# Kernel tuning notes

Hardware: AMD Instinct MI355X
Metric: run time of the kernel (lower is better)

## Reference

```python
import jax, jax.numpy as jnp
import numpy as np

B, L, D = 4, 2048, 512
H, DK, DV = 8, 64, 64


def setup_inputs() -> dict:
    key = jax.random.key(0)
    ks = jax.random.split(key, 12)
    s = 0.02
    return {
        "query": jax.random.normal(ks[0], (B, L, D), jnp.float32),
        "key": jax.random.normal(ks[1], (B, L, D), jnp.float32),
        "value": jax.random.normal(ks[2], (B, L, D), jnp.float32),
        "attention_mask": jax.random.normal(ks[3], (1, 1, L, L), jnp.float32),
        "Wq": jax.random.normal(ks[4], (D, H * DK), jnp.float32) * s,
        "bq": jnp.zeros((H * DK,), jnp.float32),
        "Wk": jax.random.normal(ks[5], (D, H * DK), jnp.float32) * s,
        "bk": jnp.zeros((H * DK,), jnp.float32),
        "Wv": jax.random.normal(ks[6], (D, H * DV), jnp.float32) * s,
        "bv": jnp.zeros((H * DV,), jnp.float32),
        "Wo": jax.random.normal(ks[7], (H * DV, D), jnp.float32) * s,
        "bo": jnp.zeros((D,), jnp.float32),
    }


def reference(query, key, value, attention_mask, Wq, bq, Wk, bk, Wv, bv, Wo, bo):
    sz_b, len_q, _ = query.shape
    len_k = key.shape[1]
    # projections -> [B, L, H, d]
    q = (query @ Wq + bq).reshape(sz_b, len_q, H, DK)
    k = (key @ Wk + bk).reshape(sz_b, len_k, H, DK)
    v = (value @ Wv + bv).reshape(sz_b, len_k, H, DV)
    # permute(2,0,1,3): heads first -> [H, B, L, d]
    q = jnp.transpose(q, (2, 0, 1, 3))
    k = jnp.transpose(k, (2, 0, 1, 3))
    v = jnp.transpose(v, (2, 0, 1, 3))
    scale = 1.0 / jnp.sqrt(jnp.asarray(DK, q.dtype))
    scores = jnp.einsum('hbqd,hbkd->hbqk', q, k) * scale + attention_mask
    attn = jax.nn.softmax(scores, axis=-1)
    x = jnp.einsum('hbqk,hbkd->hbqd', attn, v)  # [H, B, Lq, Dv]
    # faithful to torch: transpose(1,2) -> [H, Lq, B, Dv] then view(B, Lq, H*Dv)
    x = jnp.transpose(x, (0, 2, 1, 3)).reshape(sz_b, len_q, H * DV)
    return x @ Wo + bo
```

## Files before the change

### kernel.cpp

```cpp
#include <hip/hip_runtime.h>

#define SEQ    2048
#define DMODEL 512
#define NHEAD  8
#define HDIM   64
#define BATCH  4
#define NROWS  65536
#define KSPLIT 2

#define LOG2E  1.4426950408889634f
#define QSCALE 0.18033688011112042f

typedef float f32x4  __attribute__((ext_vector_type(4)));
typedef float f32x16 __attribute__((ext_vector_type(16)));
typedef _Float16 h16x8 __attribute__((ext_vector_type(8)));
typedef _Float16 h16x2 __attribute__((ext_vector_type(2)));

union U4H { uint4 u; h16x8 h; };
union U1H2 { unsigned int u; h16x2 h; };

static __device__ inline h16x2 pkrtz(float a, float b) {
    return __builtin_bit_cast(h16x2, __builtin_amdgcn_cvt_pkrtz(a, b));
}
static __device__ inline unsigned short f2h(float x) {
    _Float16 h = (_Float16)x;
    return __builtin_bit_cast(unsigned short, h);
}
static __device__ inline void async_cp16(const void* g, void* l) {
    __builtin_amdgcn_global_load_lds(
        (const __attribute__((address_space(1))) unsigned int*)g,
        (__attribute__((address_space(3))) unsigned int*)l,
        16, 0, 0);
}

__global__ __launch_bounds__(256) void transpose_cast_w(
    const float* __restrict__ s0, const float* __restrict__ s1,
    const float* __restrict__ s2, const float* __restrict__ s3,
    unsigned short* __restrict__ d0, unsigned short* __restrict__ d1,
    unsigned short* __restrict__ d2, unsigned short* __restrict__ d3)
{
    const float* S; unsigned short* D;
    switch (blockIdx.z) {
        case 0: S = s0; D = d0; break;
        case 1: S = s1; D = d1; break;
        case 2: S = s2; D = d2; break;
        default: S = s3; D = d3; break;
    }
    __shared__ float T[32][33];
    const int t = threadIdx.x;
    const int r = t >> 3, c = (t & 7) * 4;
    const int k0 = blockIdx.x * 32, n0 = blockIdx.y * 32;
    float4 v = *(const float4*)&S[(size_t)(k0 + r) * DMODEL + n0 + c];
    T[r][c] = v.x; T[r][c + 1] = v.y; T[r][c + 2] = v.z; T[r][c + 3] = v.w;
    __syncthreads();
    ushort4 o;
    o.x = f2h(T[c + 0][r]); o.y = f2h(T[c + 1][r]);
    o.z = f2h(T[c + 2][r]); o.w = f2h(T[c + 3][r]);
    *(ushort4*)&D[(size_t)(n0 + r) * DMODEL + k0 + c] = o;
}

__global__ __launch_bounds__(256) void prep_mask(
    const float* __restrict__ mask, unsigned short* __restrict__ mp)
{
    int i = blockIdx.x * 256 + threadIdx.x;
    int k = (i * 4) & (SEQ - 1);
    int q = (i * 4) >> 11;
    float4 v = ((const float4*)mask)[i];
    int kt = k >> 6, kl = k & 63;
    int mt = kl >> 5, g = (kl >> 3) & 3, hl = (kl >> 2) & 1;
    size_t base = ((size_t)kt * SEQ + q) * 64 + hl * 32 + mt * 16 + g * 4;
    ushort4 o;
    o.x = f2h(__builtin_amdgcn_exp2f(v.x * LOG2E));
    o.y = f2h(__builtin_amdgcn_exp2f(v.y * LOG2E));
    o.z = f2h(__builtin_amdgcn_exp2f(v.z * LOG2E));
    o.w = f2h(__builtin_amdgcn_exp2f(v.w * LOG2E));
    *(ushort4*)&mp[base] = o;
}

template <int A_FP32, int EPI>
static __device__ inline void gemm_core(
    const void* __restrict__ Ap, const unsigned short* __restrict__ Bt,
    const float* __restrict__ bias, void* __restrict__ Cout, float oscale,
    int bm, int bn)
{
    __shared__ __align__(16) unsigned short As[128 * 32];
    __shared__ __align__(16) unsigned short Bs[128 * 32];

    const int t = threadIdx.x;
    const int lane = t & 63, w = t >> 6;
    const int wm = w >> 1, wn = w & 1;
    const int c = lane & 15, quad = lane >> 4;

    f32x4 acc[4][4] = {};

    for (int k0 = 0; k0 < DMODEL; k0 += 32) {
        if (A_FP32) {
            const float* Af = (const float*)Ap;
            #pragma unroll
            for (int p = 0; p < 4; p++) {
                int cid = p * 256 + t;
                int row = cid >> 3, fc = cid & 7;
                float4 av = *(const float4*)&Af[(size_t)(bm + row) * DMODEL + k0 + fc * 4];
                U1H2 lo, hi;
                lo.h = pkrtz(av.x, av.y);
                hi.h = pkrtz(av.z, av.w);
                uint2 st = make_uint2(lo.u, hi.u);
                *(uint2*)&As[row * 32 + fc * 4] = st;
            }
        } else {
            const unsigned short* Ab = (const unsigned short*)Ap;
            #pragma unroll
            for (int i = 0; i < 2; i++) {
                int row = 32 * w + 16 * i + (lane >> 2);
                const unsigned short* gp = Ab + (size_t)(bm + row) * DMODEL + k0 + (lane & 3) * 8;
                async_cp16(gp, &As[(32 * w + 16 * i) * 32]);
            }
        }
        #pragma unroll
        for (int i = 0; i < 2; i++) {
            int row = 32 * w + 16 * i + (lane >> 2);
            const unsigned short* gp = Bt + (size_t)(bn + row) * DMODEL + k0 + (lane & 3) * 8;
            async_cp16(gp, &Bs[(32 * w + 16 * i) * 32]);
        }
        __syncthreads();

        U4H af[4], bf[4];
        #pragma unroll
        for (int mt = 0; mt < 4; mt++)
            af[mt].u = *(const uint4*)&As[(wm * 64 + mt * 16 + c) * 32 + quad * 8];
        #pragma unroll
        for (int nt = 0; nt < 4; nt++)
            bf[nt].u = *(const uint4*)&Bs[(wn * 64 + nt * 16 + c) * 32 + quad * 8];
        #pragma unroll
        for (int mt = 0; mt < 4; mt++)
            #pragma unroll
            for (int nt = 0; nt < 4; nt++)
                acc[mt][nt] = __builtin_amdgcn_mfma_f32_16x16x32_f16(
                    af[mt].h, bf[nt].h, acc[mt][nt], 0, 0, 0);
        __syncthreads();
    }

    if (EPI == 2) {
        #pragma unroll
        for (int nt = 0; nt < 4; nt++) {
            int ng = bn + wn * 64 + nt * 16 + c;
            int h = ng >> 6, dv = ng & 63;
            float bv = bias[ng];
            #pragma unroll
            for (int mt = 0; mt < 4; mt++) {
                int mg0 = bm + wm * 64 + mt * 16 + quad * 4;
                int bb = mg0 >> 11, key0 = mg0 & (SEQ - 1);
                U1H2 lo, hi;
                lo.h = pkrtz(acc[mt][nt][0] + bv, acc[mt][nt][1] + bv);
                hi.h = pkrtz(acc[mt][nt][2] + bv, acc[mt][nt][3] + bv);
                *(uint2*)&((unsigned short*)Cout)[
                    ((size_t)(bb * NHEAD + h) * HDIM + dv) * SEQ + key0] =
                    make_uint2(lo.u, hi.u);
            }
        }
        return;
    }
    #pragma unroll
    for (int nt = 0; nt < 4; nt++) {
        int ng = bn + wn * 64 + nt * 16 + c;
        float bv = bias[ng];
        #pragma unroll
        for (int mt = 0; mt < 4; mt++) {
            #pragma unroll
            for (int r = 0; r < 4; r++) {
                int mg = bm + wm * 64 + mt * 16 + quad * 4 + r;
                float v = (acc[mt][nt][r] + bv) * oscale;
                if (EPI == 1)
                    ((unsigned short*)Cout)[(size_t)mg * DMODEL + ng] = f2h(v);
                else
                    ((float*)Cout)[(size_t)mg * DMODEL + ng] = v;
            }
        }
    }
}

struct QKVArgs {
    const float *A0, *A1, *A2;
    const unsigned short *W0, *W1, *W2;
    const float *b0, *b1, *b2;
    unsigned short *o0, *o1, *o2;
};

__global__ __launch_bounds__(256) void gemm_qkv(QKVArgs a) {
    if (blockIdx.z == 2)
        gemm_core<1, 2>(a.A2, a.W2, a.b2, a.o2, 1.0f, blockIdx.y * 128, blockIdx.x * 128);
    else if (blockIdx.z == 1)
        gemm_core<1, 1>(a.A1, a.W1, a.b1, a.o1, 1.0f, blockIdx.y * 128, blockIdx.x * 128);
    else
        gemm_core<1, 1>(a.A0, a.W0, a.b0, a.o0, QSCALE, blockIdx.y * 128, blockIdx.x * 128);
}

__global__ __launch_bounds__(256) void gemm_fin(
    const unsigned short* __restrict__ A, const unsigned short* __restrict__ W,
    const float* __restrict__ bias, float* __restrict__ C) {
    gemm_core<0, 0>(A, W, bias, C, 1.0f, blockIdx.y * 128, blockIdx.x * 128);
}

__global__ __launch_bounds__(256, 3) void attn5(
    const unsigned short* __restrict__ qb, const unsigned short* __restrict__ kb,
    const unsigned short* __restrict__ vT, const unsigned short* __restrict__ emp,
    unsigned short* __restrict__ Xp, float* __restrict__ Lp)
{
    __shared__ __align__(16) unsigned short Ks[2][64 * 64];
    __shared__ __align__(16) unsigned short Vs[2][64 * 64];

    const int t = threadIdx.x;
    const int lane = t & 63, w = t >> 6;
    const int c32 = lane & 31, hl = lane >> 5;
    const int bh = blockIdx.x, b = bh >> 3, head = bh & 7;
    const int q0 = blockIdx.y * 128;
    const int split = blockIdx.z;
    const int qg = q0 + w * 32 + c32;

    const unsigned short* qrow = qb + ((size_t)b * SEQ + qg) * DMODEL + head * HDIM;
    U4H Qf[4];
    #pragma unroll
    for (int s = 0; s < 4; s++)
        Qf[s].u = *(const uint4*)&qrow[s * 16 + hl * 8];

    const unsigned short* kgb = kb + (size_t)b * SEQ * DMODEL + head * HDIM
                              + (size_t)split * 1024 * DMODEL;
    const unsigned short* vgb = vT + (size_t)bh * HDIM * SEQ + split * 1024;

    const int srow = lane >> 3;
    const int sch  = (lane & 7) ^ srow;

    {
        #pragma unroll
        for (int i = 0; i < 2; i++) {
            int row = w * 16 + i * 8 + srow;
            async_cp16(&kgb[(size_t)row * DMODEL + sch * 8], &Ks[0][(w * 16 + i * 8) * 64]);
            async_cp16(&vgb[(size_t)row * SEQ + sch * 8],    &Vs[0][(w * 16 + i * 8) * 64]);
        }
    }

    f32x16 O0 = {}, O1 = {};
    float lsum = 0.f;

    for (int kt = 0; kt < 1024 / 64; kt++) {
        const int p = kt & 1;
        __syncthreads();

        const int ktg = split * 16 + kt;
        const unsigned short* mrow = emp + ((size_t)ktg * SEQ + qg) * 64 + hl * 32;
        U4H e0, e1, e2, e3;
        e0.u = *(const uint4*)&mrow[0];
        e1.u = *(const uint4*)&mrow[8];
        e2.u = *(const uint4*)&mrow[16];
        e3.u = *(const uint4*)&mrow[24];

        if (kt + 1 < 1024 / 64) {
            int k0n = (kt + 1) * 64;
            #pragma unroll
            for (int i = 0; i < 2; i++) {
                int row = w * 16 + i * 8 + srow;
                async_cp16(&kgb[(size_t)(k0n + row) * DMODEL + sch * 8],
                           &Ks[p ^ 1][(w * 16 + i * 8) * 64]);
                async_cp16(&vgb[(size_t)row * SEQ + k0n + sch * 8],
                           &Vs[p ^ 1][(w * 16 + i * 8) * 64]);
            }
        }

        const unsigned short* Kp = Ks[p];
        const unsigned short* Vp = Vs[p];

        f32x16 S0 = {}, S1 = {};
        #pragma unroll
        for (int s = 0; s < 4; s++) {
            int fc = 2 * s + hl;
            int sl = (fc ^ (c32 & 7)) * 8;
            U4H ka0, ka1;
            ka0.u = *(const uint4*)&Kp[c32 * 64 + sl];
            ka1.u = *(const uint4*)&Kp[(32 + c32) * 64 + sl];
            S0 = __builtin_amdgcn_mfma_f32_32x32x16_f16(ka0.h, Qf[s].h, S0, 0, 0, 0);
            S1 = __builtin_amdgcn_mfma_f32_32x32x16_f16(ka1.h, Qf[s].h, S1, 0, 0, 0);
        }

        unsigned int Pf[4][4];
        #pragma unroll
        for (int mt = 0; mt < 2; mt++) {
            f32x16 S = mt ? S1 : S0;
            h16x8 ea = (mt ? e2 : e0).h;
            h16x8 eb = (mt ? e3 : e1).h;
            unsigned int u[4][2];
            #pragma unroll
            for (int jj = 0; jj < 8; jj++) {
                _Float16 exl = (jj < 4) ? ea[2 * jj]     : eb[2 * jj - 8];
                _Float16 exh = (jj < 4) ? ea[2 * jj + 1] : eb[2 * jj - 7];
                h16x2 ex = {exl, exh};
                h16x2 pk = pkrtz(__builtin_amdgcn_exp2f(S[2 * jj]),
                                 __builtin_amdgcn_exp2f(S[2 * jj + 1]));
                h16x2 pp = pk * ex;
                lsum += (float)pp[0] + (float)pp[1];
                u[jj >> 1][jj & 1] = __builtin_bit_cast(unsigned int, pp);
            }
            unsigned int sA0 = hl ? u[0][0] : u[1][0];
            unsigned int sA1 = hl ? u[0][1] : u[1][1];
            unsigned int sB0 = hl ? u[2][0] : u[3][0];
            unsigned int sB1 = hl ? u[2][1] : u[3][1];
            unsigned int rA0 = (unsigned)__shfl_xor((int)sA0, 32, 64);
            unsigned int rA1 = (unsigned)__shfl_xor((int)sA1, 32, 64);
            unsigned int rB0 = (unsigned)__shfl_xor((int)sB0, 32, 64);
            unsigned int rB1 = (unsigned)__shfl_xor((int)sB1, 32, 64);
            Pf[2 * mt + 0][0] = hl ? rA0 : u[0][0];
            Pf[2 * mt + 0][1] = hl ? rA1 : u[0][1];
            Pf[2 * mt + 0][2] = hl ? u[1][0] : rA0;
            Pf[2 * mt + 0][3] = hl ? u[1][1] : rA1;
            Pf[2 * mt + 1][0] = hl ? rB0 : u[2][0];
            Pf[2 * mt + 1][1] = hl ? rB1 : u[2][1];
            Pf[2 * mt + 1][2] = hl ? u[3][0] : rB0;
            Pf[2 * mt + 1][3] = hl ? u[3][1] : rB1;
        }

        #pragma unroll
        for (int s = 0; s < 4; s++) {
            int kc = 2 * s + hl;
            int sl = (kc ^ (c32 & 7)) * 8;
            U4H va0, va1, pu;
            va0.u = *(const uint4*)&Vp[c32 * 64 + sl];
            va1.u = *(const uint4*)&Vp[(32 + c32) * 64 + sl];
            pu.u = make_uint4(Pf[s][0], Pf[s][1], Pf[s][2], Pf[s][3]);
            O0 = __builtin_amdgcn_mfma_f32_32x32x16_f16(va0.h, pu.h, O0, 0, 0, 0);
            O1 = __builtin_amdgcn_mfma_f32_32x32x16_f16(va1.h, pu.h, O1, 0, 0, 0);
        }
    }

    lsum += __shfl_xor(lsum, 32, 64);
    const size_t j = ((size_t)head * SEQ + qg) * BATCH + b;
    unsigned short* xr = Xp + ((size_t)split * NROWS + j) * HDIM;
    #pragma unroll
    for (int mt = 0; mt < 2; mt++) {
        f32x16 Ov = mt ? O1 : O0;
        #pragma unroll
        for (int g = 0; g < 4; g++) {
            U1H2 lo, hi;
            lo.h = pkrtz(Ov[g * 4 + 0], Ov[g * 4 + 1]);
            hi.h = pkrtz(Ov[g * 4 + 2], Ov[g * 4 + 3]);
            uint2 st = make_uint2(lo.u, hi.u);
            *(uint2*)&xr[mt * 32 + 8 * g + 4 * hl] = st;
        }
    }
    if (hl == 0) Lp[split * NROWS + j] = lsum;
}

__global__ __launch_bounds__(256) void combine_attn(
    const unsigned short* __restrict__ Xp, const float* __restrict__ Lp,
    unsigned short* __restrict__ xb)
{
    int i = blockIdx.x * 256 + threadIdx.x;
    int j = i >> 3, dc = (i & 7) * 8;
    U4H a, b;
    a.u = *(const uint4*)&Xp[(size_t)j * HDIM + dc];
    b.u = *(const uint4*)&Xp[((size_t)NROWS + j) * HDIM + dc];
    float inv = 1.0f / (Lp[j] + Lp[NROWS + j]);
    U4H o;
    #pragma unroll
    for (int p = 0; p < 4; p++) {
        float s0 = ((float)a.h[2 * p]     + (float)b.h[2 * p])     * inv;
        float s1 = ((float)a.h[2 * p + 1] + (float)b.h[2 * p + 1]) * inv;
        h16x2 pk = pkrtz(s0, s1);
        o.h[2 * p] = pk[0]; o.h[2 * p + 1] = pk[1];
    }
    *(uint4*)&xb[(size_t)j * HDIM + dc] = o.u;
}

extern "C" void kernel_launch(void* const* d_in, const int* in_sizes, int n_in,
                              void* d_out, int out_size, void* d_ws, size_t ws_size,
                              hipStream_t stream) {
    const float* query = (const float*)d_in[0];
    const float* key_  = (const float*)d_in[1];
    const float* value = (const float*)d_in[2];
    const float* mask  = (const float*)d_in[3];
    const float* Wq = (const float*)d_in[4];
    const float* bq = (const float*)d_in[5];
    const float* Wk = (const float*)d_in[6];
    const float* bk = (const float*)d_in[7];
    const float* Wv = (const float*)d_in[8];
    const float* bv = (const float*)d_in[9];
    const float* Wo = (const float*)d_in[10];
    const float* bo = (const float*)d_in[11];
    float* out = (float*)d_out;

    const size_t NP = (size_t)BATCH * SEQ * DMODEL;
    unsigned short* ws   = (unsigned short*)d_ws;
    unsigned short* qb16 = ws;
    unsigned short* kb16 = qb16 + NP;
    unsigned short* vT16 = kb16 + NP;
    unsigned short* xb16 = vT16 + NP;
    unsigned short* em16 = xb16 + NP;
    unsigned short* Xp16 = em16 + (size_t)SEQ * SEQ;
    unsigned short* WqT  = Xp16 + (size_t)KSPLIT * NROWS * HDIM;
    unsigned short* WkT  = WqT + DMODEL * DMODEL;
    unsigned short* WvT  = WkT + DMODEL * DMODEL;
    unsigned short* WoT  = WvT + DMODEL * DMODEL;
    float* Lp = (float*)(WoT + DMODEL * DMODEL);

    transpose_cast_w<<<dim3(16, 16, 4), 256, 0, stream>>>(
        Wq, Wk, Wv, Wo, WqT, WkT, WvT, WoT);
    prep_mask<<<dim3(SEQ * SEQ / 4 / 256), 256, 0, stream>>>(mask, em16);

    QKVArgs qa;
    qa.A0 = query; qa.A1 = key_; qa.A2 = value;
    qa.W0 = WqT;   qa.W1 = WkT;  qa.W2 = WvT;
    qa.b0 = bq;    qa.b1 = bk;   qa.b2 = bv;
    qa.o0 = qb16;  qa.o1 = kb16; qa.o2 = vT16;
    gemm_qkv<<<dim3(DMODEL / 128, BATCH * SEQ / 128, 3), 256, 0, stream>>>(qa);

    attn5<<<dim3(BATCH * NHEAD, SEQ / 128, KSPLIT), 256, 0, stream>>>(
        qb16, kb16, vT16, em16, Xp16, Lp);

    combine_attn<<<dim3(NROWS * 8 / 256), 256, 0, stream>>>(Xp16, Lp, xb16);

    gemm_fin<<<dim3(DMODEL / 128, BATCH * SEQ / 128), 256, 0, stream>>>(
        xb16, WoT, bo, out);
}
```

Baseline: 253.1 us.

## Double-buffer GEMM tiles, repack LDS layouts, shrink output GEMM tile, coalesce mask prep

The shared GEMM core gains a double-buffered LDS pipeline. The next K-tile is prefetched (async copies, or fp32 register loads converted after the MFMAs) while the current one is computed, with one barrier per iteration and a padded k-chunk-major LDS layout. The output projection GEMM now uses 64-row tiles with a 3-wave occupancy hint so more blocks run, and the QKV GEMM gets a 2-block occupancy hint. The attention kernel replaces its XOR-swizzled K/V LDS tiles with a padded chunk-major layout, and the mask prep kernel is reindexed so reads are row-contiguous. These changes add LDS use and register pressure in exchange for hiding global-load latency and avoiding bank conflicts.

```diff
diff --git a/kernel.cpp b/kernel.cpp
--- a/kernel.cpp
+++ b/kernel.cpp
@@ -62,82 +62,124 @@
 __global__ __launch_bounds__(256) void prep_mask(
     const float* __restrict__ mask, unsigned short* __restrict__ mp)
 {
-    int i = blockIdx.x * 256 + threadIdx.x;
-    int k = (i * 4) & (SEQ - 1);
-    int q = (i * 4) >> 11;
-    float4 v = ((const float4*)mask)[i];
-    int kt = k >> 6, kl = k & 63;
-    int mt = kl >> 5, g = (kl >> 3) & 3, hl = (kl >> 2) & 1;
-    size_t base = ((size_t)kt * SEQ + q) * 64 + hl * 32 + mt * 16 + g * 4;
-    ushort4 o;
-    o.x = f2h(__builtin_amdgcn_exp2f(v.x * LOG2E));
-    o.y = f2h(__builtin_amdgcn_exp2f(v.y * LOG2E));
-    o.z = f2h(__builtin_amdgcn_exp2f(v.z * LOG2E));
-    o.w = f2h(__builtin_amdgcn_exp2f(v.w * LOG2E));
-    *(ushort4*)&mp[base] = o;
-}
-
-template <int A_FP32, int EPI>
+    const int t = threadIdx.x;
+    const int kt = blockIdx.x;
+    const int q  = blockIdx.y * 16 + (t >> 4);
+    const int l  = t & 15;
+    const int hl = l >> 3, mt = (l >> 2) & 1, g = l & 3;
+    const int f4 = kt * 16 + 8 * mt + 2 * g + hl;
+    float4 v = ((const float4*)mask)[(size_t)q * (SEQ / 4) + f4];
+    U1H2 lo, hi;
+    lo.h = pkrtz(__builtin_amdgcn_exp2f(v.x * LOG2E),
+                 __builtin_amdgcn_exp2f(v.y * LOG2E));
+    hi.h = pkrtz(__builtin_amdgcn_exp2f(v.z * LOG2E),
+                 __builtin_amdgcn_exp2f(v.w * LOG2E));
+    *(uint2*)&mp[((size_t)kt * SEQ + q) * 64 + l * 4] = make_uint2(lo.u, hi.u);
+}
+
+template <int A_FP32, int EPI, int BM>
 static __device__ inline void gemm_core(
     const void* __restrict__ Ap, const unsigned short* __restrict__ Bt,
     const float* __restrict__ bias, void* __restrict__ Cout, float oscale,
     int bm, int bn)
 {
-    __shared__ __align__(16) unsigned short As[128 * 32];
-    __shared__ __align__(16) unsigned short Bs[128 * 32];
+    const int ACS = BM * 8 + 8;
+    const int MT  = BM / 32;
+    __shared__ __align__(16) unsigned short As[2][4 * (BM * 8 + 8)];
+    __shared__ __align__(16) unsigned short Bs[2][4 * 1032];
 
     const int t = threadIdx.x;
     const int lane = t & 63, w = t >> 6;
     const int wm = w >> 1, wn = w & 1;
     const int c = lane & 15, quad = lane >> 4;
 
-    f32x4 acc[4][4] = {};
-
-    for (int k0 = 0; k0 < DMODEL; k0 += 32) {
-        if (A_FP32) {
-            const float* Af = (const float*)Ap;
-            #pragma unroll
-            for (int p = 0; p < 4; p++) {
-                int cid = p * 256 + t;
-                int row = cid >> 3, fc = cid & 7;
-                float4 av = *(const float4*)&Af[(size_t)(bm + row) * DMODEL + k0 + fc * 4];
-                U1H2 lo, hi;
-                lo.h = pkrtz(av.x, av.y);
-                hi.h = pkrtz(av.z, av.w);
-                uint2 st = make_uint2(lo.u, hi.u);
-                *(uint2*)&As[row * 32 + fc * 4] = st;
-            }
-        } else {
-            const unsigned short* Ab = (const unsigned short*)Ap;
-            #pragma unroll
-            for (int i = 0; i < 2; i++) {
-                int row = 32 * w + 16 * i + (lane >> 2);
-                const unsigned short* gp = Ab + (size_t)(bm + row) * DMODEL + k0 + (lane & 3) * 8;
-                async_cp16(gp, &As[(32 * w + 16 * i) * 32]);
-            }
-        }
-        #pragma unroll
-        for (int i = 0; i < 2; i++) {
-            int row = 32 * w + 16 * i + (lane >> 2);
-            const unsigned short* gp = Bt + (size_t)(bn + row) * DMODEL + k0 + (lane & 3) * 8;
-            async_cp16(gp, &Bs[(32 * w + 16 * i) * 32]);
-        }
+    const unsigned short* Ab = (const unsigned short*)Ap;
+    const float* Af = (const float*)Ap;
+
+    f32x4 acc[MT][4] = {};
+    float4 areg[BM / 32];
+
+    if (A_FP32) {
+        #pragma unroll
+        for (int p = 0; p < BM / 32; p++) {
+            int cid = p * 256 + t;
+            int row = cid >> 3, fc4 = cid & 7;
+            float4 av = *(const float4*)&Af[(size_t)(bm + row) * DMODEL + fc4 * 4];
+            U1H2 lo, hi;
+            lo.h = pkrtz(av.x, av.y); hi.h = pkrtz(av.z, av.w);
+            *(uint2*)&As[0][(fc4 >> 1) * ACS + row * 8 + (fc4 & 1) * 4] =
+                make_uint2(lo.u, hi.u);
+        }
+    } else {
+        #pragma unroll
+        for (int h = 0; h < BM / 64; h++) {
+            int row = h * 64 + lane;
+            async_cp16(&Ab[(size_t)(bm + row) * DMODEL + w * 8],
+                       &As[0][w * ACS + h * 512]);
+        }
+    }
+    #pragma unroll
+    for (int h = 0; h < 2; h++) {
+        int row = h * 64 + lane;
+        async_cp16(&Bt[(size_t)(bn + row) * DMODEL + w * 8],
+                   &Bs[0][w * 1032 + h * 512]);
+    }
+
+    for (int kt = 0; kt < DMODEL / 32; kt++) {
+        const int p = kt & 1;
         __syncthreads();
 
-        U4H af[4], bf[4];
-        #pragma unroll
-        for (int mt = 0; mt < 4; mt++)
-            af[mt].u = *(const uint4*)&As[(wm * 64 + mt * 16 + c) * 32 + quad * 8];
+        const int kn = (kt + 1) * 32;
+        if (kt + 1 < DMODEL / 32) {
+            if (A_FP32) {
+                #pragma unroll
+                for (int pp = 0; pp < BM / 32; pp++) {
+                    int cid = pp * 256 + t;
+                    int row = cid >> 3, fc4 = cid & 7;
+                    areg[pp] = *(const float4*)&Af[(size_t)(bm + row) * DMODEL + kn + fc4 * 4];
+                }
+            } else {
+                #pragma unroll
+                for (int h = 0; h < BM / 64; h++) {
+                    int row = h * 64 + lane;
+                    async_cp16(&Ab[(size_t)(bm + row) * DMODEL + kn + w * 8],
+                               &As[p ^ 1][w * ACS + h * 512]);
+                }
+            }
+            #pragma unroll
+            for (int h = 0; h < 2; h++) {
+                int row = h * 64 + lane;
+                async_cp16(&Bt[(size_t)(bn + row) * DMODEL + kn + w * 8],
+                           &Bs[p ^ 1][w * 1032 + h * 512]);
+            }
+        }
+
+        U4H af[MT], bf[4];
+        #pragma unroll
+        for (int mt = 0; mt < MT; mt++)
+            af[mt].u = *(const uint4*)&As[p][quad * ACS + (wm * (BM / 2) + mt * 16 + c) * 8];
         #pragma unroll
         for (int nt = 0; nt < 4; nt++)
-            bf[nt].u = *(const uint4*)&Bs[(wn * 64 + nt * 16 + c) * 32 + quad * 8];
-        #pragma unroll
-        for (int mt = 0; mt < 4; mt++)
+            bf[nt].u = *(const uint4*)&Bs[p][quad * 1032 + (wn * 64 + nt * 16 + c) * 8];
+        #pragma unroll
+        for (int mt = 0; mt < MT; mt++)
             #pragma unroll
             for (int nt = 0; nt < 4; nt++)
                 acc[mt][nt] = __builtin_amdgcn_mfma_f32_16x16x32_f16(
                     af[mt].h, bf[nt].h, acc[mt][nt], 0, 0, 0);
-        __syncthreads();
+
+        if (A_FP32 && kt + 1 < DMODEL / 32) {
+            #pragma unroll
+            for (int pp = 0; pp < BM / 32; pp++) {
+                int cid = pp * 256 + t;
+                int row = cid >> 3, fc4 = cid & 7;
+                U1H2 lo, hi;
+                lo.h = pkrtz(areg[pp].x, areg[pp].y);
+                hi.h = pkrtz(areg[pp].z, areg[pp].w);
+                *(uint2*)&As[p ^ 1][(fc4 >> 1) * ACS + row * 8 + (fc4 & 1) * 4] =
+                    make_uint2(lo.u, hi.u);
+            }
+        }
     }
 
     if (EPI == 2) {
@@ -147,8 +189,8 @@
             int h = ng >> 6, dv = ng & 63;
             float bv = bias[ng];
             #pragma unroll
-            for (int mt = 0; mt < 4; mt++) {
-                int mg0 = bm + wm * 64 + mt * 16 + quad * 4;
+            for (int mt = 0; mt < MT; mt++) {
+                int mg0 = bm + wm * (BM / 2) + mt * 16 + quad * 4;
                 int bb = mg0 >> 11, key0 = mg0 & (SEQ - 1);
                 U1H2 lo, hi;
                 lo.h = pkrtz(acc[mt][nt][0] + bv, acc[mt][nt][1] + bv);
@@ -165,10 +207,10 @@
         int ng = bn + wn * 64 + nt * 16 + c;
         float bv = bias[ng];
         #pragma unroll
-        for (int mt = 0; mt < 4; mt++) {
+        for (int mt = 0; mt < MT; mt++) {
             #pragma unroll
             for (int r = 0; r < 4; r++) {
-                int mg = bm + wm * 64 + mt * 16 + quad * 4 + r;
+                int mg = bm + wm * (BM / 2) + mt * 16 + quad * 4 + r;
                 float v = (acc[mt][nt][r] + bv) * oscale;
                 if (EPI == 1)
                     ((unsigned short*)Cout)[(size_t)mg * DMODEL + ng] = f2h(v);
@@ -186,28 +228,27 @@
     unsigned short *o0, *o1, *o2;
 };
 
-__global__ __launch_bounds__(256) void gemm_qkv(QKVArgs a) {
+__global__ __launch_bounds__(256, 2) void gemm_qkv(QKVArgs a) {
     if (blockIdx.z == 2)
-        gemm_core<1, 2>(a.A2, a.W2, a.b2, a.o2, 1.0f, blockIdx.y * 128, blockIdx.x * 128);
+        gemm_core<1, 2, 128>(a.A2, a.W2, a.b2, a.o2, 1.0f, blockIdx.y * 128, blockIdx.x * 128);
     else if (blockIdx.z == 1)
-        gemm_core<1, 1>(a.A1, a.W1, a.b1, a.o1, 1.0f, blockIdx.y * 128, blockIdx.x * 128);
+        gemm_core<1, 1, 128>(a.A1, a.W1, a.b1, a.o1, 1.0f, blockIdx.y * 128, blockIdx.x * 128);
     else
-        gemm_core<1, 1>(a.A0, a.W0, a.b0, a.o0, QSCALE, blockIdx.y * 128, blockIdx.x * 128);
-}
-
-__global__ __launch_bounds__(256) void gemm_fin(
+        gemm_core<1, 1, 128>(a.A0, a.W0, a.b0, a.o0, QSCALE, blockIdx.y * 128, blockIdx.x * 128);
+}
+
+__global__ __launch_bounds__(256, 3) void gemm_fin(
     const unsigned short* __restrict__ A, const unsigned short* __restrict__ W,
     const float* __restrict__ bias, float* __restrict__ C) {
-    gemm_core<0, 0>(A, W, bias, C, 1.0f, blockIdx.y * 128, blockIdx.x * 128);
-}
-
-__global__ __launch_bounds__(256, 3) void attn5(
+    gemm_core<0, 0, 64>(A, W, bias, C, 1.0f, blockIdx.y * 64, blockIdx.x * 128);
+}
+
+__global__ __launch_bounds__(256, 3) void attn6(
     const unsigned short* __restrict__ qb, const unsigned short* __restrict__ kb,
     const unsigned short* __restrict__ vT, const unsigned short* __restrict__ emp,
     unsigned short* __restrict__ Xp, float* __restrict__ Lp)
 {
-    __shared__ __align__(16) unsigned short Ks[2][64 * 64];
-    __shared__ __align__(16) unsigned short Vs[2][64 * 64];
+    __shared__ __align__(16) unsigned short KV[2][2][8 * 520];
 
     const int t = threadIdx.x;
     const int lane = t & 63, w = t >> 6;
@@ -216,6 +257,7 @@
     const int q0 = blockIdx.y * 128;
     const int split = blockIdx.z;
     const int qg = q0 + w * 32 + c32;
+    const int NT = (SEQ / KSPLIT) / 64;
 
     const unsigned short* qrow = qb + ((size_t)b * SEQ + qg) * DMODEL + head * HDIM;
     U4H Qf[4];
@@ -224,29 +266,24 @@
         Qf[s].u = *(const uint4*)&qrow[s * 16 + hl * 8];
 
     const unsigned short* kgb = kb + (size_t)b * SEQ * DMODEL + head * HDIM
-                              + (size_t)split * 1024 * DMODEL;
-    const unsigned short* vgb = vT + (size_t)bh * HDIM * SEQ + split * 1024;
-
-    const int srow = lane >> 3;
-    const int sch  = (lane & 7) ^ srow;
-
-    {
-        #pragma unroll
-        for (int i = 0; i < 2; i++) {
-            int row = w * 16 + i * 8 + srow;
-            async_cp16(&kgb[(size_t)row * DMODEL + sch * 8], &Ks[0][(w * 16 + i * 8) * 64]);
-            async_cp16(&vgb[(size_t)row * SEQ + sch * 8],    &Vs[0][(w * 16 + i * 8) * 64]);
-        }
+                              + (size_t)split * (SEQ / KSPLIT) * DMODEL;
+    const unsigned short* vgb = vT + (size_t)bh * HDIM * SEQ + split * (SEQ / KSPLIT);
+
+    #pragma unroll
+    for (int i = 0; i < 2; i++) {
+        int fc = 2 * w + i;
+        async_cp16(&kgb[(size_t)lane * DMODEL + fc * 8], &KV[0][0][fc * 520]);
+        async_cp16(&vgb[(size_t)lane * SEQ + fc * 8],    &KV[0][1][fc * 520]);
     }
 
     f32x16 O0 = {}, O1 = {};
     float lsum = 0.f;
 
-    for (int kt = 0; kt < 1024 / 64; kt++) {
+    for (int kt = 0; kt < NT; kt++) {
         const int p = kt & 1;
         __syncthreads();
 
-        const int ktg = split * 16 + kt;
+        const int ktg = split * NT + kt;
         const unsigned short* mrow = emp + ((size_t)ktg * SEQ + qg) * 64 + hl * 32;
         U4H e0, e1, e2, e3;
         e0.u = *(const uint4*)&mrow[0];
@@ -254,29 +291,28 @@
         e2.u = *(const uint4*)&mrow[16];
         e3.u = *(const uint4*)&mrow[24];
 
-        if (kt + 1 < 1024 / 64) {
+        if (kt + 1 < NT) {
             int k0n = (kt + 1) * 64;
             #pragma unroll
             for (int i = 0; i < 2; i++) {
-                int row = w * 16 + i * 8 + srow;
-                async_cp16(&kgb[(size_t)(k0n + row) * DMODEL + sch * 8],
-                           &Ks[p ^ 1][(w * 16 + i * 8) * 64]);
-                async_cp16(&vgb[(size_t)row * SEQ + k0n + sch * 8],
-                           &Vs[p ^ 1][(w * 16 + i * 8) * 64]);
-            }
-        }
-
-        const unsigned short* Kp = Ks[p];
-        const unsigned short* Vp = Vs[p];
+                int fc = 2 * w + i;
+                async_cp16(&kgb[(size_t)(k0n + lane) * DMODEL + fc * 8],
+                           &KV[p ^ 1][0][fc * 520]);
+                async_cp16(&vgb[(size_t)lane * SEQ + k0n + fc * 8],
+                           &KV[p ^ 1][1][fc * 520]);
+            }
+        }
+
+        const unsigned short* Kp = KV[p][0];
+        const unsigned short* Vp = KV[p][1];
 
         f32x16 S0 = {}, S1 = {};
         #pragma unroll
         for (int s = 0; s < 4; s++) {
             int fc = 2 * s + hl;
-            int sl = (fc ^ (c32 & 7)) * 8;
             U4H ka0, ka1;
-            ka0.u = *(const uint4*)&Kp[c32 * 64 + sl];
-            ka1.u = *(const uint4*)&Kp[(32 + c32) * 64 + sl];
+            ka0.u = *(const uint4*)&Kp[(fc * 65 + c32) * 8];
+            ka1.u = *(const uint4*)&Kp[(fc * 65 + 32 + c32) * 8];
             S0 = __builtin_amdgcn_mfma_f32_32x32x16_f16(ka0.h, Qf[s].h, S0, 0, 0, 0);
             S1 = __builtin_amdgcn_mfma_f32_32x32x16_f16(ka1.h, Qf[s].h, S1, 0, 0, 0);
         }
@@ -320,10 +356,9 @@
         #pragma unroll
         for (int s = 0; s < 4; s++) {
             int kc = 2 * s + hl;
-            int sl = (kc ^ (c32 & 7)) * 8;
             U4H va0, va1, pu;
-            va0.u = *(const uint4*)&Vp[c32 * 64 + sl];
-            va1.u = *(const uint4*)&Vp[(32 + c32) * 64 + sl];
+            va0.u = *(const uint4*)&Vp[(kc * 65 + c32) * 8];
+            va1.u = *(const uint4*)&Vp[(kc * 65 + 32 + c32) * 8];
             pu.u = make_uint4(Pf[s][0], Pf[s][1], Pf[s][2], Pf[s][3]);
             O0 = __builtin_amdgcn_mfma_f32_32x32x16_f16(va0.h, pu.h, O0, 0, 0, 0);
             O1 = __builtin_amdgcn_mfma_f32_32x32x16_f16(va1.h, pu.h, O1, 0, 0, 0);
@@ -402,7 +437,7 @@
 
     transpose_cast_w<<<dim3(16, 16, 4), 256, 0, stream>>>(
         Wq, Wk, Wv, Wo, WqT, WkT, WvT, WoT);
-    prep_mask<<<dim3(SEQ * SEQ / 4 / 256), 256, 0, stream>>>(mask, em16);
+    prep_mask<<<dim3(SEQ / 64, SEQ / 16), 256, 0, stream>>>(mask, em16);
 
     QKVArgs qa;
     qa.A0 = query; qa.A1 = key_; qa.A2 = value;
@@ -411,11 +446,11 @@
     qa.o0 = qb16;  qa.o1 = kb16; qa.o2 = vT16;
     gemm_qkv<<<dim3(DMODEL / 128, BATCH * SEQ / 128, 3), 256, 0, stream>>>(qa);
 
-    attn5<<<dim3(BATCH * NHEAD, SEQ / 128, KSPLIT), 256, 0, stream>>>(
+    attn6<<<dim3(BATCH * NHEAD, SEQ / 128, KSPLIT), 256, 0, stream>>>(
         qb16, kb16, vT16, em16, Xp16, Lp);
 
     combine_attn<<<dim3(NROWS * 8 / 256), 256, 0, stream>>>(Xp16, Lp, xb16);
 
-    gemm_fin<<<dim3(DMODEL / 128, BATCH * SEQ / 128), 256, 0, stream>>>(
+    gemm_fin<<<dim3(DMODEL / 128, BATCH * SEQ / 64), 256, 0, stream>>>(
         xb16, WoT, bo, out);
 }
```

After: 273.1 us. +7.9%, slower.
